# Performance work log

Hardware: AMD Instinct MI355X
Metric: run time of the kernel (lower is better)

## Reference

```python
import jax, jax.numpy as jnp
import numpy as np

NUM_HEAD = 16
NUM_SEQ = 2048
NUM_FEAT = 1024
HEAD_DIM = NUM_FEAT // NUM_HEAD
LN_EPS = 1e-5


def _constants():
    # decay per head: log(1 - 2^{-5-h})
    decay = jnp.log(1.0 - 2.0 ** (-5.0 - jnp.arange(NUM_HEAD, dtype=jnp.float32)))
    idx = jnp.arange(NUM_SEQ, dtype=jnp.float32)
    diff = idx[:, None] - idx[None, :]                      # [s, s]
    # exp(diff * decay) on lower triangle (incl. diagonal), 0 above
    mask = jnp.where(diff[None] >= 0, jnp.exp(diff[None] * decay[:, None, None]), 0.0)  # [h, s, s]
    # rotary angles: each frequency repeated twice
    angle = 1.0 / 10000.0 ** jnp.linspace(0.0, 1.0, HEAD_DIM // 2)
    angle = jnp.repeat(angle, 2)                            # [hd]
    sin = jnp.sin(idx[:, None] * angle[None, :])            # [s, hd]
    cos = jnp.cos(idx[:, None] * angle[None, :])
    return mask, sin, cos


def _rotate_every_two(x):
    x1 = x[..., ::2]
    x2 = x[..., 1::2]
    return jnp.stack((-x2, x1), axis=-1).reshape(x.shape)


def setup_inputs() -> dict:
    key = jax.random.key(0)
    ks = jax.random.split(key, 5)
    b, s, d = 4, NUM_SEQ, NUM_FEAT
    x = jax.random.normal(ks[0], (b, s, d), dtype=jnp.float32)
    Wq = jax.random.normal(ks[1], (d, d), dtype=jnp.float32) * 0.02
    Wk = jax.random.normal(ks[2], (d, d), dtype=jnp.float32) * 0.02
    Wv = jax.random.normal(ks[3], (d, d), dtype=jnp.float32) * 0.02
    Wo = jax.random.normal(ks[4], (d, d), dtype=jnp.float32) * 0.02
    ln_w = jnp.ones((HEAD_DIM,), dtype=jnp.float32)
    ln_b = jnp.zeros((HEAD_DIM,), dtype=jnp.float32)
    return {"x": x, "Wq": Wq, "Wk": Wk, "Wv": Wv, "Wo": Wo, "ln_w": ln_w, "ln_b": ln_b}


def reference(x, Wq, Wk, Wv, Wo, ln_w, ln_b):
    b, s, d = x.shape
    h, hd = NUM_HEAD, HEAD_DIM
    mask, sin, cos = _constants()

    def proj(W):
        # torch Linear (no bias): x @ W.T -> [b, h, s, hd]
        return (x @ W.T).reshape(b, s, h, hd).transpose(0, 2, 1, 3)

    q, k, v = proj(Wq), proj(Wk), proj(Wv)
    # rotary theta shift (sin/cos broadcast over batch & head)
    q = q * cos + _rotate_every_two(q) * sin
    k = k * cos + _rotate_every_two(k) * sin

    r = jnp.einsum('bhsd,bhtd->bhst', q, k) * mask[None]    # decay-masked scores
    o = jnp.einsum('bhst,bhtd->bhsd', r, v)                 # [b, h, s, hd]

    # LayerNorm over head_dim
    mu = jnp.mean(o, axis=-1, keepdims=True)
    var = jnp.var(o, axis=-1, keepdims=True)
    y = (o - mu) * jax.lax.rsqrt(var + LN_EPS) * ln_w + ln_b

    y = y.transpose(0, 2, 1, 3).reshape(b, s, d)
    return jax.nn.silu(y) @ Wo.T
```

## Files before the change

### kernel.cpp

```cpp
#include <hip/hip_runtime.h>
#include <math.h>

typedef unsigned short u16;
typedef __attribute__((ext_vector_type(8))) short short8;
typedef __attribute__((ext_vector_type(4))) float floatx4;

#define LDS_AS(p) ((__attribute__((address_space(3))) void*)(p))
#define GLB_AS(p) ((const __attribute__((address_space(1))) void*)(p))

__device__ __forceinline__ u16 f2bf(float f) {
  unsigned int u = __float_as_uint(f);
  u += 0x7fffu + ((u >> 16) & 1u);
  return (u16)(u >> 16);
}

__device__ __forceinline__ void gld16(const void* g, void* l) {
  __builtin_amdgcn_global_load_lds(GLB_AS(g), LDS_AS(l), 16, 0, 0);
}

__device__ __forceinline__ floatx4 mfma16(short8 a, short8 b, floatx4 c) {
  return __builtin_amdgcn_mfma_f32_16x16x32_bf16(a, b, c, 0, 0, 0);
}

__global__ void prep_kernel(const float* __restrict__ x, const float* __restrict__ Wq,
                            const float* __restrict__ Wk, const float* __restrict__ Wv,
                            const float* __restrict__ Wo, u16* __restrict__ xp,
                            u16* __restrict__ wqkvp, u16* __restrict__ wop,
                            float2* __restrict__ rtab) {
  int i = blockIdx.x * blockDim.x + threadIdx.x;
  const int str = gridDim.x * blockDim.x;
  for (; i < 3211264; i += str) {
    if (i < 3145728) {
      int U; u16* d;
      const float* s;
      if (i < 2097152)      { U = i;           d = xp;    s = x;  }
      else if (i < 2883584) { U = i - 2097152; d = wqkvp; s = nullptr; }
      else                  { U = i - 2883584; d = wop;   s = Wo; }
      const int tile = U >> 12;
      const int kc   = (U >> 7) & 31;
      const int lane = (U >> 1) & 63;
      const int jh   = U & 1;
      const int scol = kc * 32 + (lane >> 4) * 8 + jh * 4;
      int srow = tile * 16 + (lane & 15);
      if (s == nullptr) {
        const int sel = srow >> 10;
        srow &= 1023;
        s = (sel == 0) ? Wq : (sel == 1) ? Wk : Wv;
      }
      float4 v = ((const float4*)s)[srow * 256 + (scol >> 2)];
      ushort4 o;
      o.x = f2bf(v.x); o.y = f2bf(v.y); o.z = f2bf(v.z); o.w = f2bf(v.w);
      ((ushort4*)d)[U] = o;
    } else {
      const int t = i - 3145728;
      const int seq = t >> 5, dh = t & 31;
      const float freq = exp2f(-(float)dh * 0.42863594770f);
      float sn, cs;
      __sincosf((float)seq * freq, &sn, &cs);
      rtab[t] = make_float2(sn, cs);
    }
  }
}

template <int EPI>
__global__ __launch_bounds__(512, 2)
void gemm_bt(const u16* __restrict__ A, const u16* __restrict__ Bw, int K,
             u16* __restrict__ qb, u16* __restrict__ kb, u16* __restrict__ vtb,
             u16* __restrict__ kwt, const float2* __restrict__ rtab,
             float* __restrict__ outp) {
  __shared__ __align__(16) u16 smem[65536];
  const int tid = threadIdx.x;
  const int w = tid >> 6, lane = tid & 63;
  const int quad = lane >> 4, l15 = lane & 15;
  const int wr = w >> 2, wc = w & 3;
  const int m0 = blockIdx.y * 256, n0 = blockIdx.x * 256;

  const size_t tsz = (size_t)(K >> 5) * 512;
  const u16* A0 = A + ((size_t)(m0 >> 4) + 2 * w) * tsz + lane * 8;
  const u16* A1 = A0 + tsz;
  const u16* B0 = Bw + ((size_t)(n0 >> 4) + 2 * w) * tsz + lane * 8;
  const u16* B1 = B0 + tsz;

  auto stage = [&](int buf, int kc) {
    const int nb = buf * 16384;
    gld16(A0 + (size_t)kc * 512, &smem[nb + (2 * w) * 512]);
    gld16(A1 + (size_t)kc * 512, &smem[nb + (2 * w + 1) * 512]);
    gld16(B0 + (size_t)kc * 512, &smem[nb + 8192 + (2 * w) * 512]);
    gld16(B1 + (size_t)kc * 512, &smem[nb + 8192 + (2 * w + 1) * 512]);
  };

  floatx4 acc[8][4] = {};
  const int NT = K >> 5;

  stage(0, 0);
  stage(1, 1);
  stage(2, 2);

  for (int t = 0; t < NT; ++t) {
    if (t <= NT - 3)
      asm volatile("s_waitcnt vmcnt(8)" ::: "memory");
    else if (t == NT - 2)
      asm volatile("s_waitcnt vmcnt(4)" ::: "memory");
    else
      asm volatile("s_waitcnt vmcnt(0)" ::: "memory");
    __builtin_amdgcn_s_barrier();
    asm volatile("" ::: "memory");
    __builtin_amdgcn_sched_barrier(0);

    if (t + 3 < NT) stage((t + 3) & 3, t + 3);

    const u16* Ap = &smem[(t & 3) * 16384];
    const u16* Bp = Ap + 8192;
    short8 a[8], b[4];
#pragma unroll
    for (int i = 0; i < 8; ++i)
      a[i] = *(const short8*)&Ap[(wr * 8 + i) * 512 + lane * 8];
#pragma unroll
    for (int j = 0; j < 4; ++j)
      b[j] = *(const short8*)&Bp[(wc * 4 + j) * 512 + lane * 8];
    __builtin_amdgcn_s_setprio(1);
#pragma unroll
    for (int i = 0; i < 8; ++i)
#pragma unroll
      for (int j = 0; j < 4; ++j)
        acc[i][j] = mfma16(a[i], b[j], acc[i][j]);
    __builtin_amdgcn_s_setprio(0);
    asm volatile("" ::: "memory");
  }
  __builtin_amdgcn_s_barrier();

  u16* scr = &smem[w * 4096];

  const int ncb = n0 + wc * 64;
  const int lr = lane >> 3, lc = lane & 7;

#pragma unroll
  for (int ih = 0; ih < 2; ++ih) {
    const int mrb = m0 + wr * 128 + ih * 64;

    if (EPI == 0) {
      const int which = n0 >> 10;
      const int c1024 = ncb & 1023;
      const int bidx = mrb >> 11;
      const int hh = c1024 >> 6;
      const int seq0 = mrb & 2047;

      if (which < 2) {
#pragma unroll
        for (int j = 0; j < 4; ++j) {
          const int d = j * 16 + l15;
          const int dc = d >> 3, dl = d & 7;
#pragma unroll
          for (int i = 0; i < 4; ++i)
#pragma unroll
            for (int r = 0; r < 4; ++r) {
              const int sl = i * 16 + quad * 4 + r;
              const int seq = seq0 + sl;
              const float v = acc[ih * 4 + i][j][r];
              const float p = __shfl_xor(v, 1, 64);
              const float2 sc = rtab[(d >> 1) + seq * 32];
              const float res = (d & 1) ? (v * sc.y + p * sc.x) : (v * sc.y - p * sc.x);
              scr[sl * 64 + (((dc + (sl >> 2)) & 7) << 3) + dl] = f2bf(res);
            }
        }
        u16* dst = ((which == 0) ? qb : kb) + (size_t)(bidx * 16 + hh) * 131072 +
                   (size_t)seq0 * 64;
#pragma unroll
        for (int cch = 0; cch < 8; ++cch) {
          const int row = cch * 8 + lr;
          const int slot = (lc + (row >> 2)) & 7;
          short8 vv = *(const short8*)&scr[row * 64 + slot * 8];
          *(short8*)(dst + (size_t)row * 64 + lc * 8) = vv;
        }
        if (which == 1) {
          const float l2h = __log2f(1.0f - exp2f(-(float)(5 + hh)));
#pragma unroll
          for (int j = 0; j < 4; ++j) {
            const int d = j * 16 + l15;
#pragma unroll
            for (int i = 0; i < 4; ++i) {
              ushort4 pk;
#pragma unroll
              for (int r = 0; r < 4; ++r) {
                const int sl = i * 16 + quad * 4 + r;
                const int seq = seq0 + sl;
                const float v = acc[ih * 4 + i][j][r];
                const float p = __shfl_xor(v, 1, 64);
                const float2 sc = rtab[(d >> 1) + seq * 32];
                const float res = (d & 1) ? (v * sc.y + p * sc.x) : (v * sc.y - p * sc.x);
                const float wgt = exp2f((float)(127 - (seq & 127)) * l2h);
                ((u16*)&pk)[r] = f2bf(res * wgt);
              }
              *(ushort4*)&scr[d * 64 + ((i * 16 + quad * 4 + 8 * (d & 7)) & 63)] = pk;
            }
          }
          u16* dw = kwt + (size_t)(bidx * 16 + hh) * 131072 + seq0;
#pragma unroll
          for (int cch = 0; cch < 8; ++cch) {
            const int drow = cch * 8 + lr;
            const int slot = (lc + (drow & 7)) & 7;
            short8 vv = *(const short8*)&scr[drow * 64 + slot * 8];
            *(short8*)(dw + (size_t)drow * 2048 + lc * 8) = vv;
          }
        }
      } else {
#pragma unroll
        for (int j = 0; j < 4; ++j) {
          const int d = j * 16 + l15;
#pragma unroll
          for (int i = 0; i < 4; ++i) {
            ushort4 pk;
            pk.x = f2bf(acc[ih * 4 + i][j][0]);
            pk.y = f2bf(acc[ih * 4 + i][j][1]);
            pk.z = f2bf(acc[ih * 4 + i][j][2]);
            pk.w = f2bf(acc[ih * 4 + i][j][3]);
            *(ushort4*)&scr[d * 64 + ((i * 16 + quad * 4 + 8 * (d & 7)) & 63)] = pk;
          }
        }
        u16* dh = vtb + (size_t)(bidx * 16 + hh) * 131072 + seq0;
#pragma unroll
        for (int cch = 0; cch < 8; ++cch) {
          const int drow = cch * 8 + lr;
          const int slot = (lc + (drow & 7)) & 7;
          short8 vv = *(const short8*)&scr[drow * 64 + slot * 8];
          *(short8*)(dh + (size_t)drow * 2048 + lc * 8) = vv;
        }
      }
    } else {
      float* scrf = (float*)scr;
      const int lr4 = lane >> 4, lc16 = lane & 15;
#pragma unroll
      for (int p = 0; p < 4; ++p) {
#pragma unroll
        for (int j = 0; j < 4; ++j)
#pragma unroll
          for (int r = 0; r < 4; ++r)
            scrf[(quad * 4 + r) * 65 + j * 16 + l15] = acc[ih * 4 + p][j][r];
#pragma unroll
        for (int cch = 0; cch < 4; ++cch) {
          const int rr = cch * 4 + lr4;
          float4 vv = *(const float4*)&scrf[rr * 65 + lc16 * 4];
          *(float4*)&outp[(size_t)(mrb + p * 16 + rr) * 1024 + ncb + lc16 * 4] = vv;
        }
      }
    }
  }
}

__global__ __launch_bounds__(256, 4)
void kvchunk_kernel(const u16* __restrict__ kwt, const u16* __restrict__ vtb,
                    float* __restrict__ U) {
  __shared__ __align__(16) u16 kls[16 * 512];
  __shared__ __align__(16) u16 vls[16 * 512];
  const int c = blockIdx.x, bh = blockIdx.y;
  const int tid = threadIdx.x, w = tid >> 6, lane = tid & 63;
  const int quad = lane >> 4, l15 = lane & 15;
  const u16* kg = kwt + (size_t)bh * 131072 + c * 128;
  const u16* vg = vtb + (size_t)bh * 131072 + c * 128;
#pragma unroll
  for (int rg = 0; rg < 4; ++rg) {
    const int rid = w * 4 + rg;
    const int m = rid >> 2, kst = rid & 3;
    gld16(kg + (size_t)(m * 16 + l15) * 2048 + kst * 32 + quad * 8, &kls[rid * 512]);
    gld16(vg + (size_t)(m * 16 + l15) * 2048 + kst * 32 + quad * 8, &vls[rid * 512]);
  }
  __syncthreads();
  floatx4 acc[4] = {};
#pragma unroll
  for (int kst = 0; kst < 4; ++kst) {
    short8 bf = *(const short8*)&vls[(w * 4 + kst) * 512 + lane * 8];
#pragma unroll
    for (int m = 0; m < 4; ++m) {
      short8 af = *(const short8*)&kls[(m * 4 + kst) * 512 + lane * 8];
      acc[m] = mfma16(af, bf, acc[m]);
    }
  }
  float* Ub = U + ((size_t)bh * 16 + c) * 4096;
#pragma unroll
  for (int m = 0; m < 4; ++m)
#pragma unroll
    for (int r = 0; r < 4; ++r)
      Ub[(m * 16 + quad * 4 + r) * 64 + w * 16 + l15] = acc[m][r];
}

__global__ void scan_kernel(const float* __restrict__ U, u16* __restrict__ Sb) {
  const int bh = blockIdx.x;
  const int w = threadIdx.x >> 6, l = threadIdx.x & 63;
  const int h = bh & 15;
  const float l2 = __log2f(1.0f - exp2f(-(float)(5 + h)));
  const float lamL = exp2f(128.0f * l2);
  float S[16];
#pragma unroll
  for (int i = 0; i < 16; ++i) S[i] = 0.f;
  for (int c = 0; c < 16; ++c) {
    u16* sp = Sb + ((size_t)bh * 16 + c) * 4096 + l * 64 + w * 16;
#pragma unroll
    for (int dk = 0; dk < 16; dk += 4) {
      ushort4 pk;
      pk.x = f2bf(S[dk]);     pk.y = f2bf(S[dk + 1]);
      pk.z = f2bf(S[dk + 2]); pk.w = f2bf(S[dk + 3]);
      *(ushort4*)&sp[dk] = pk;
    }
    const float* up = U + ((size_t)bh * 16 + c) * 4096 + (w * 16) * 64 + l;
#pragma unroll
    for (int dk = 0; dk < 16; ++dk)
      S[dk] = lamL * S[dk] + up[dk * 64];
  }
}

__global__ __launch_bounds__(256, 2)
void attn_chunk_kernel(const u16* __restrict__ qb, const u16* __restrict__ kb,
                       const u16* __restrict__ vtb, const u16* __restrict__ Sb,
                       const float* __restrict__ lnw, const float* __restrict__ lnb,
                       u16* __restrict__ yb) {
  __shared__ __align__(16) u16 kls[16 * 512];
  __shared__ __align__(16) u16 vls[16 * 512];
  __shared__ __align__(16) u16 Sls[8 * 512];
  __shared__ __align__(16) u16 pls[4 * 32 * 40];

  const int c = blockIdx.x, bh = blockIdx.y, h = bh & 15;
  const int tid = threadIdx.x;
  const int w = tid >> 6, lane = tid & 63, quad = lane >> 4, l15 = lane & 15;
  const float l2 = __log2f(1.0f - exp2f(-(float)(5 + h)));

  const u16* kg = kb + (size_t)bh * 131072 + (size_t)c * 128 * 64;
  const u16* vg = vtb + (size_t)bh * 131072 + (size_t)c * 128;
  const u16* Sg = Sb + ((size_t)bh * 16 + c) * 4096;
#pragma unroll
  for (int rg = 0; rg < 4; ++rg) {
    const int kid = w * 4 + rg;
    const int nsub = kid >> 1, kk = kid & 1;
    gld16(kg + (size_t)(nsub * 16 + l15) * 64 + kk * 32 + quad * 8, &kls[kid * 512]);
    const int jd = kid >> 2, kst = kid & 3;
    gld16(vg + (size_t)(jd * 16 + l15) * 2048 + kst * 32 + quad * 8, &vls[kid * 512]);
  }
#pragma unroll
  for (int e = 0; e < 2; ++e) {
    const int rid = w * 2 + e;
    const int nd = rid >> 1, kk = rid & 1;
    gld16(Sg + (size_t)(nd * 16 + l15) * 64 + kk * 32 + quad * 8, &Sls[rid * 512]);
  }

  short8 qf[2][2];
  {
    const u16* qbase = qb + ((size_t)bh * 2048 + c * 128 + w * 32 + l15) * 64 + quad * 8;
#pragma unroll
    for (int i = 0; i < 2; ++i)
#pragma unroll
      for (int kk = 0; kk < 2; ++kk)
        qf[i][kk] = *(const short8*)(qbase + (size_t)i * 16 * 64 + kk * 32);
  }
  float lnwv[4], lnbv[4];
#pragma unroll
  for (int jd = 0; jd < 4; ++jd) {
    lnwv[jd] = lnw[jd * 16 + l15];
    lnbv[jd] = lnb[jd * 16 + l15];
  }
  __syncthreads();

  floatx4 sacc[2][8] = {};
#pragma unroll
  for (int kk = 0; kk < 2; ++kk) {
    short8 bf[8];
#pragma unroll
    for (int j = 0; j < 8; ++j)
      bf[j] = *(const short8*)&kls[(j * 2 + kk) * 512 + lane * 8];
#pragma unroll
    for (int i = 0; i < 2; ++i)
#pragma unroll
      for (int j = 0; j < 8; ++j)
        sacc[i][j] = mfma16(qf[i][kk], bf[j], sacc[i][j]);
  }

  floatx4 oacc[2][4] = {};
#pragma unroll
  for (int kk = 0; kk < 2; ++kk)
#pragma unroll
    for (int nd = 0; nd < 4; ++nd) {
      short8 sf = *(const short8*)&Sls[(nd * 2 + kk) * 512 + lane * 8];
#pragma unroll
      for (int i = 0; i < 2; ++i)
        oacc[i][nd] = mfma16(qf[i][kk], sf, oacc[i][nd]);
    }
  float rowf[8];
#pragma unroll
  for (int i = 0; i < 2; ++i)
#pragma unroll
    for (int r = 0; r < 4; ++r)
      rowf[i * 4 + r] = exp2f((float)(w * 32 + i * 16 + quad * 4 + r) * l2);
  const float lam1 = exp2f(l2);
#pragma unroll
  for (int i = 0; i < 2; ++i)
#pragma unroll
    for (int nd = 0; nd < 4; ++nd)
#pragma unroll
      for (int r = 0; r < 4; ++r)
        oacc[i][nd][r] *= rowf[i * 4 + r] * lam1;

  float colf[8];
#pragma unroll
  for (int j = 0; j < 8; ++j) colf[j] = exp2f(-(float)(j * 16 + l15) * l2);
  u16* pw = &pls[w * 1280];
#pragma unroll
  for (int kst = 0; kst < 4; ++kst) {
#pragma unroll
    for (int jl = 0; jl < 2; ++jl) {
      const int j = kst * 2 + jl;
#pragma unroll
      for (int i = 0; i < 2; ++i)
#pragma unroll
        for (int r = 0; r < 4; ++r) {
          const int srow = i * 16 + quad * 4 + r;
          const int dlt = (w * 32 + srow) - (j * 16 + l15);
          const float v =
              (dlt >= 0) ? sacc[i][j][r] * rowf[i * 4 + r] * colf[j] : 0.0f;
          pw[srow * 40 + jl * 16 + l15] = f2bf(v);
        }
    }
    short8 pf[2], vf[4];
#pragma unroll
    for (int i = 0; i < 2; ++i)
      pf[i] = *(const short8*)&pw[(i * 16 + l15) * 40 + quad * 8];
#pragma unroll
    for (int jd = 0; jd < 4; ++jd)
      vf[jd] = *(const short8*)&vls[(jd * 4 + kst) * 512 + lane * 8];
#pragma unroll
    for (int i = 0; i < 2; ++i)
#pragma unroll
      for (int jd = 0; jd < 4; ++jd)
        oacc[i][jd] = mfma16(pf[i], vf[jd], oacc[i][jd]);
  }

  __syncthreads();
  u16* scrw = &kls[w * 2048];
  const int b = bh >> 4;
#pragma unroll
  for (int i = 0; i < 2; ++i)
#pragma unroll
    for (int r = 0; r < 4; ++r) {
      float sum = 0.f, ssq = 0.f;
#pragma unroll
      for (int jd = 0; jd < 4; ++jd) {
        const float v = oacc[i][jd][r];
        sum += v;
        ssq += v * v;
      }
#pragma unroll
      for (int off = 1; off < 16; off <<= 1) {
        sum += __shfl_xor(sum, off, 64);
        ssq += __shfl_xor(ssq, off, 64);
      }
      const float mu = sum * (1.0f / 64.0f);
      const float var = ssq * (1.0f / 64.0f) - mu * mu;
      const float rst = rsqrtf(var + 1e-5f);
      const int sl = i * 16 + quad * 4 + r;
#pragma unroll
      for (int jd = 0; jd < 4; ++jd) {
        const float z = (oacc[i][jd][r] - mu) * rst * lnwv[jd] + lnbv[jd];
        const float y = z / (1.0f + expf(-z));
        const int f = jd * 16 + l15;
        scrw[sl * 64 + ((((f >> 3) + (sl >> 2)) & 7) << 3) + (f & 7)] = f2bf(y);
      }
    }
  const int tile0 = b * 128 + c * 8 + w * 2;
#pragma unroll
  for (int tt = 0; tt < 2; ++tt)
#pragma unroll
    for (int kcl = 0; kcl < 2; ++kcl) {
      const int row = tt * 16 + l15;
      const int slot = ((kcl * 4 + quad) + (row >> 2)) & 7;
      short8 vv = *(const short8*)&scrw[row * 64 + slot * 8];
      *(short8*)(yb + ((size_t)(tile0 + tt) * 32 + h * 2 + kcl) * 512 + lane * 8) = vv;
    }
}

extern "C" void kernel_launch(void* const* d_in, const int* in_sizes, int n_in,
                              void* d_out, int out_size, void* d_ws, size_t ws_size,
                              hipStream_t stream) {
  const float* x   = (const float*)d_in[0];
  const float* Wq  = (const float*)d_in[1];
  const float* Wk  = (const float*)d_in[2];
  const float* Wv  = (const float*)d_in[3];
  const float* Wo  = (const float*)d_in[4];
  const float* lnw = (const float*)d_in[5];
  const float* lnb = (const float*)d_in[6];
  float* out = (float*)d_out;

  char* ws = (char*)d_ws;
  u16* xbf  = (u16*)(ws + 0);
  u16* wqkv = (u16*)(ws + 16777216);
  u16* Sb   = (u16*)(ws + 16777216);
  u16* qbuf = (u16*)(ws + 25165824);
  u16* kbuf = (u16*)(ws + 41943040);
  u16* vtb  = (u16*)(ws + 58720256);
  u16* wo   = (u16*)(ws + 75497472);
  float2* rtab = (float2*)(ws + 77594624);
  u16* yb   = xbf;
  u16* kwt  = (u16*)d_out;
  float* Ubuf = (float*)((char*)d_out + 16777216);

  prep_kernel<<<dim3(1024), dim3(256), 0, stream>>>(x, Wq, Wk, Wv, Wo, xbf, wqkv, wo,
                                                    rtab);
  gemm_bt<0><<<dim3(12, 32), dim3(512), 0, stream>>>(xbf, wqkv, 1024, qbuf, kbuf, vtb,
                                                     kwt, rtab, nullptr);
  kvchunk_kernel<<<dim3(16, 64), dim3(256), 0, stream>>>(kwt, vtb, Ubuf);
  scan_kernel<<<dim3(64), dim3(256), 0, stream>>>(Ubuf, Sb);
  attn_chunk_kernel<<<dim3(16, 64), dim3(256), 0, stream>>>(qbuf, kbuf, vtb, Sb, lnw,
                                                            lnb, yb);
  gemm_bt<1><<<dim3(4, 32), dim3(512), 0, stream>>>(yb, wo, 1024, nullptr, nullptr,
                                                    nullptr, nullptr, nullptr, out);
}
```

Measured before the change: 266.4 us.

## Shrink GEMM block tiles to 256 threads and switch to triple-buffered LDS

Both GEMM instantiations now use 256-thread blocks with smaller M tiles: 128x256 for the QKV projection and 64x256 for the output projection. This multiplies the grid size (768 and 512 blocks) so more CUs stay busy. The LDS pipeline drops from four buffers with a prefetch distance of three to three buffers with a distance of two, which cuts shared memory per block. The cost is lower operand reuse per block and a shallower prefetch that may expose more load latency.

```diff
diff --git a/kernel.cpp b/kernel.cpp
--- a/kernel.cpp
+++ b/kernel.cpp
@@ -63,80 +63,90 @@
 }
 
 template <int EPI>
-__global__ __launch_bounds__(512, 2)
+__global__ __launch_bounds__(256, 2)
 void gemm_bt(const u16* __restrict__ A, const u16* __restrict__ Bw, int K,
              u16* __restrict__ qb, u16* __restrict__ kb, u16* __restrict__ vtb,
              u16* __restrict__ kwt, const float2* __restrict__ rtab,
              float* __restrict__ outp) {
-  __shared__ __align__(16) u16 smem[65536];
+  constexpr int AP   = (EPI == 0) ? 8 : 4;
+  constexpr int BUFU = (AP + 16) * 512;
+  constexpr int AOFF = AP * 512;
+  constexpr int AI   = (EPI == 0) ? 8 : 4;
+  constexpr int IH   = (EPI == 0) ? 2 : 1;
+  __shared__ __align__(16) u16 smem[3 * 12288];
   const int tid = threadIdx.x;
   const int w = tid >> 6, lane = tid & 63;
   const int quad = lane >> 4, l15 = lane & 15;
-  const int wr = w >> 2, wc = w & 3;
-  const int m0 = blockIdx.y * 256, n0 = blockIdx.x * 256;
+  const int m0 = blockIdx.y * (EPI == 0 ? 128 : 64), n0 = blockIdx.x * 256;
 
   const size_t tsz = (size_t)(K >> 5) * 512;
-  const u16* A0 = A + ((size_t)(m0 >> 4) + 2 * w) * tsz + lane * 8;
+  const u16* A0 = A + ((size_t)(m0 >> 4) + (EPI == 0 ? 2 * w : w)) * tsz + lane * 8;
   const u16* A1 = A0 + tsz;
-  const u16* B0 = Bw + ((size_t)(n0 >> 4) + 2 * w) * tsz + lane * 8;
-  const u16* B1 = B0 + tsz;
+  const u16* Bb = Bw + ((size_t)(n0 >> 4) + 4 * w) * tsz + lane * 8;
 
   auto stage = [&](int buf, int kc) {
-    const int nb = buf * 16384;
-    gld16(A0 + (size_t)kc * 512, &smem[nb + (2 * w) * 512]);
-    gld16(A1 + (size_t)kc * 512, &smem[nb + (2 * w + 1) * 512]);
-    gld16(B0 + (size_t)kc * 512, &smem[nb + 8192 + (2 * w) * 512]);
-    gld16(B1 + (size_t)kc * 512, &smem[nb + 8192 + (2 * w + 1) * 512]);
+    const int nb = buf * BUFU;
+    gld16(A0 + (size_t)kc * 512, &smem[nb + (EPI == 0 ? 2 * w : w) * 512]);
+    if constexpr (EPI == 0)
+      gld16(A1 + (size_t)kc * 512, &smem[nb + (2 * w + 1) * 512]);
+#pragma unroll
+    for (int e = 0; e < 4; ++e)
+      gld16(Bb + (size_t)e * tsz + (size_t)kc * 512,
+            &smem[nb + AOFF + (4 * w + e) * 512]);
   };
 
-  floatx4 acc[8][4] = {};
+  floatx4 acc[AI][4] = {};
   const int NT = K >> 5;
 
   stage(0, 0);
   stage(1, 1);
-  stage(2, 2);
-
+
+  int cur = 0, stg = 2;
   for (int t = 0; t < NT; ++t) {
-    if (t <= NT - 3)
-      asm volatile("s_waitcnt vmcnt(8)" ::: "memory");
-    else if (t == NT - 2)
-      asm volatile("s_waitcnt vmcnt(4)" ::: "memory");
-    else
+    if (t + 1 < NT) {
+      if constexpr (EPI == 0)
+        asm volatile("s_waitcnt vmcnt(6)" ::: "memory");
+      else
+        asm volatile("s_waitcnt vmcnt(5)" ::: "memory");
+    } else {
       asm volatile("s_waitcnt vmcnt(0)" ::: "memory");
+    }
     __builtin_amdgcn_s_barrier();
     asm volatile("" ::: "memory");
     __builtin_amdgcn_sched_barrier(0);
 
-    if (t + 3 < NT) stage((t + 3) & 3, t + 3);
-
-    const u16* Ap = &smem[(t & 3) * 16384];
-    const u16* Bp = Ap + 8192;
-    short8 a[8], b[4];
-#pragma unroll
-    for (int i = 0; i < 8; ++i)
-      a[i] = *(const short8*)&Ap[(wr * 8 + i) * 512 + lane * 8];
+    if (t + 2 < NT) stage(stg, t + 2);
+
+    const u16* Ap = &smem[cur * BUFU];
+    const u16* Bp = Ap + AOFF;
+    short8 a[AI], b[4];
+#pragma unroll
+    for (int i = 0; i < AI; ++i)
+      a[i] = *(const short8*)&Ap[i * 512 + lane * 8];
 #pragma unroll
     for (int j = 0; j < 4; ++j)
-      b[j] = *(const short8*)&Bp[(wc * 4 + j) * 512 + lane * 8];
+      b[j] = *(const short8*)&Bp[(w * 4 + j) * 512 + lane * 8];
     __builtin_amdgcn_s_setprio(1);
 #pragma unroll
-    for (int i = 0; i < 8; ++i)
+    for (int i = 0; i < AI; ++i)
 #pragma unroll
       for (int j = 0; j < 4; ++j)
         acc[i][j] = mfma16(a[i], b[j], acc[i][j]);
     __builtin_amdgcn_s_setprio(0);
     asm volatile("" ::: "memory");
+    cur = (cur == 2) ? 0 : cur + 1;
+    stg = (stg == 2) ? 0 : stg + 1;
   }
   __builtin_amdgcn_s_barrier();
 
   u16* scr = &smem[w * 4096];
 
-  const int ncb = n0 + wc * 64;
+  const int ncb = n0 + w * 64;
   const int lr = lane >> 3, lc = lane & 7;
 
 #pragma unroll
-  for (int ih = 0; ih < 2; ++ih) {
-    const int mrb = m0 + wr * 128 + ih * 64;
+  for (int ih = 0; ih < IH; ++ih) {
+    const int mrb = m0 + ih * 64;
 
     if (EPI == 0) {
       const int which = n0 >> 10;
@@ -235,7 +245,7 @@
         for (int j = 0; j < 4; ++j)
 #pragma unroll
           for (int r = 0; r < 4; ++r)
-            scrf[(quad * 4 + r) * 65 + j * 16 + l15] = acc[ih * 4 + p][j][r];
+            scrf[(quad * 4 + r) * 65 + j * 16 + l15] = acc[p][j][r];
 #pragma unroll
         for (int cch = 0; cch < 4; ++cch) {
           const int rr = cch * 4 + lr4;
@@ -501,12 +511,12 @@
 
   prep_kernel<<<dim3(1024), dim3(256), 0, stream>>>(x, Wq, Wk, Wv, Wo, xbf, wqkv, wo,
                                                     rtab);
-  gemm_bt<0><<<dim3(12, 32), dim3(512), 0, stream>>>(xbf, wqkv, 1024, qbuf, kbuf, vtb,
+  gemm_bt<0><<<dim3(12, 64), dim3(256), 0, stream>>>(xbf, wqkv, 1024, qbuf, kbuf, vtb,
                                                      kwt, rtab, nullptr);
   kvchunk_kernel<<<dim3(16, 64), dim3(256), 0, stream>>>(kwt, vtb, Ubuf);
   scan_kernel<<<dim3(64), dim3(256), 0, stream>>>(Ubuf, Sb);
   attn_chunk_kernel<<<dim3(16, 64), dim3(256), 0, stream>>>(qbuf, kbuf, vtb, Sb, lnw,
                                                             lnb, yb);
-  gemm_bt<1><<<dim3(4, 32), dim3(512), 0, stream>>>(yb, wo, 1024, nullptr, nullptr,
-                                                    nullptr, nullptr, nullptr, out);
-}
+  gemm_bt<1><<<dim3(4, 128), dim3(256), 0, stream>>>(yb, wo, 1024, nullptr, nullptr,
+                                                     nullptr, nullptr, nullptr, out);
+}
```

New measurement: 243.8 us. 1.09x faster.
